# Kernel optimization log

Measured on AMD Instinct MI355X. Metric: run time of the kernel, lower is better.

Reference implementation:

```python
import jax, jax.numpy as jnp
import numpy as np

IN_CH = 4096
OUT_CH = 4096
NNZ = 838860
BATCH = 16384


def setup_inputs() -> dict:
    key = jax.random.key(0)
    k_x, k_w, k_b, k_r, k_c = jax.random.split(key, 5)
    x = jax.random.normal(k_x, (BATCH, IN_CH), dtype=jnp.float32)
    sparse_weight = jax.random.normal(k_w, (NNZ,), dtype=jnp.float32)
    bias = jax.random.normal(k_b, (OUT_CH,), dtype=jnp.float32)
    rows = jax.random.randint(k_r, (NNZ,), 0, OUT_CH, dtype=jnp.int32)
    cols = jax.random.randint(k_c, (NNZ,), 0, IN_CH, dtype=jnp.int32)
    return {"x": x, "sparse_weight": sparse_weight, "bias": bias, "rows": rows, "cols": cols}


def reference(x, sparse_weight, bias, rows, cols):
    # Scatter sparse weights into dense [OUT_CH, IN_CH] buffer (zero elsewhere),
    # exactly mirroring the torch module's per-call zero-fill + fancy-index assign.
    dense_weight = jnp.zeros((OUT_CH, IN_CH), dtype=sparse_weight.dtype)
    dense_weight = dense_weight.at[rows, cols].set(sparse_weight)
    # (W @ x.T).T + b  ==  x @ W.T + b
    return jnp.einsum('ni,oi->no', x, dense_weight) + bias
```

## Files before the change

kernel.cpp:

```cpp
#include <hip/hip_runtime.h>

#define IN_CH 4096
#define OUT_CH 4096
#define BATCH 16384

typedef __attribute__((ext_vector_type(8))) short bf16x8;
typedef __attribute__((ext_vector_type(4))) float f32x4;
typedef __attribute__((ext_vector_type(8))) unsigned short us8;

__device__ __forceinline__ unsigned short f2bf(float f) {
    union { float f; unsigned int u; } v; v.f = f;
    unsigned int u = v.u;
    unsigned int r = (u + 0x7fffu + ((u >> 16) & 1u)) >> 16;
    return (unsigned short)r;
}

__global__ void scatter_max(const int* __restrict__ rows, const int* __restrict__ cols,
                            int* __restrict__ idx, int nnz) {
    int i = blockIdx.x * blockDim.x + threadIdx.x;
    if (i < nnz) {
        atomicMax(&idx[(size_t)rows[i] * IN_CH + cols[i]], i + 1);
    }
}

__global__ void scatter_write(const int* __restrict__ rows, const int* __restrict__ cols,
                              const float* __restrict__ w, const int* __restrict__ idx,
                              unsigned short* __restrict__ W, int nnz) {
    int i = blockIdx.x * blockDim.x + threadIdx.x;
    if (i < nnz) {
        size_t cell = (size_t)rows[i] * IN_CH + cols[i];
        if (idx[cell] == i + 1) W[cell] = f2bf(w[i]);
    }
}

__global__ void convert_x(const float* __restrict__ x, unsigned short* __restrict__ xb) {
    size_t i = ((size_t)blockIdx.x * blockDim.x + threadIdx.x) * 8;
    float4 f0 = *(const float4*)(x + i);
    float4 f1 = *(const float4*)(x + i + 4);
    us8 o;
    o[0] = f2bf(f0.x); o[1] = f2bf(f0.y); o[2] = f2bf(f0.z); o[3] = f2bf(f0.w);
    o[4] = f2bf(f1.x); o[5] = f2bf(f1.y); o[6] = f2bf(f1.z); o[7] = f2bf(f1.w);
    *(us8*)(xb + i) = o;
}

__device__ __forceinline__ void gl_lds16(const unsigned short* g, unsigned short* l) {
    __builtin_amdgcn_global_load_lds(
        (const __attribute__((address_space(1))) unsigned int*)g,
        (__attribute__((address_space(3))) unsigned int*)l,
        16, 0, 0);
}

__global__ __launch_bounds__(256) void gemm_bt(
    const unsigned short* __restrict__ A,
    const unsigned short* __restrict__ B,
    const float* __restrict__ bias,
    float* __restrict__ C)
{
    __shared__ unsigned short lds[8192];
    const int tid  = threadIdx.x;
    const int wave = tid >> 6;
    const int lane = tid & 63;
    const int bm = blockIdx.x >> 5;
    const int bn = blockIdx.x & 31;
    const int wm = wave & 1;
    const int wn = wave >> 1;
    const int ml   = lane & 15;
    const int quad = lane >> 4;
    const int srow = lane >> 2;
    const int c    = lane & 3;
    const int scol = (c ^ ((srow >> 1) & 3)) * 8;

    const int seg0 = wave * 2;
    const unsigned short* ga0 = A + (size_t)(bm * 128 + seg0 * 16 + srow) * IN_CH + scol;
    const unsigned short* ga1 = ga0 + 16 * IN_CH;
    const unsigned short* gb0 = B + (size_t)(bn * 128 + seg0 * 16 + srow) * IN_CH + scol;
    const unsigned short* gb1 = gb0 + 16 * IN_CH;
    unsigned short* la0 = lds + seg0 * 512;
    unsigned short* la1 = la0 + 512;
    unsigned short* lb0 = lds + 4096 + seg0 * 512;
    unsigned short* lb1 = lb0 + 512;

    f32x4 acc[4][4];
#pragma unroll
    for (int i = 0; i < 4; ++i)
#pragma unroll
        for (int j = 0; j < 4; ++j) acc[i][j] = (f32x4){0.f, 0.f, 0.f, 0.f};

    const unsigned short* ldsA = lds;
    const unsigned short* ldsB = lds + 4096;
    const int swk = (quad ^ ((ml >> 1) & 3)) * 8;

    for (int kt = 0; kt < IN_CH / 32; ++kt) {
        gl_lds16(ga0, la0);
        gl_lds16(ga1, la1);
        gl_lds16(gb0, lb0);
        gl_lds16(gb1, lb1);
        __syncthreads();

        bf16x8 af[4], bf[4];
#pragma unroll
        for (int mt = 0; mt < 4; ++mt)
            af[mt] = *(const bf16x8*)(ldsA + (size_t)(wm * 64 + mt * 16 + ml) * 32 + swk);
#pragma unroll
        for (int nt = 0; nt < 4; ++nt)
            bf[nt] = *(const bf16x8*)(ldsB + (size_t)(wn * 64 + nt * 16 + ml) * 32 + swk);

#pragma unroll
        for (int mt = 0; mt < 4; ++mt)
#pragma unroll
            for (int nt = 0; nt < 4; ++nt)
                acc[mt][nt] = __builtin_amdgcn_mfma_f32_16x16x32_bf16(
                    af[mt], bf[nt], acc[mt][nt], 0, 0, 0);

        __syncthreads();
        ga0 += 32; ga1 += 32; gb0 += 32; gb1 += 32;
    }

    const int gm0 = bm * 128 + wm * 64;
    const int gn0 = bn * 128 + wn * 64;
#pragma unroll
    for (int nt = 0; nt < 4; ++nt) {
        const int gn = gn0 + nt * 16 + ml;
        const float bv = bias[gn];
#pragma unroll
        for (int mt = 0; mt < 4; ++mt) {
            const int gm = gm0 + mt * 16 + quad * 4;
#pragma unroll
            for (int r = 0; r < 4; ++r)
                C[(size_t)(gm + r) * OUT_CH + gn] = acc[mt][nt][r] + bv;
        }
    }
}

extern "C" void kernel_launch(void* const* d_in, const int* in_sizes, int n_in,
                              void* d_out, int out_size, void* d_ws, size_t ws_size,
                              hipStream_t stream) {
    const float* x    = (const float*)d_in[0];
    const float* sw   = (const float*)d_in[1];
    const float* bias = (const float*)d_in[2];
    const int*   rows = (const int*)d_in[3];
    const int*   cols = (const int*)d_in[4];
    const int    nnz  = in_sizes[1];

    char* base = (char*)d_ws;
    unsigned short* W  = (unsigned short*)base;
    int*            idx = (int*)(base + (size_t)OUT_CH * IN_CH * 2);
    unsigned short* xb  = (unsigned short*)(base + (size_t)OUT_CH * IN_CH * 2);

    hipMemsetAsync(d_ws, 0, (size_t)OUT_CH * IN_CH * 2 + (size_t)OUT_CH * IN_CH * 4, stream);
    hipLaunchKernelGGL(scatter_max, dim3((nnz + 255) / 256), dim3(256), 0, stream,
                       rows, cols, idx, nnz);
    hipLaunchKernelGGL(scatter_write, dim3((nnz + 255) / 256), dim3(256), 0, stream,
                       rows, cols, sw, idx, W, nnz);
    hipLaunchKernelGGL(convert_x, dim3(32768), dim3(256), 0, stream, x, xb);
    hipLaunchKernelGGL(gemm_bt, dim3(4096), dim3(256), 0, stream, xb, W, bias, (float*)d_out);
}
```

Before: 1.112 ms.

## Rewrite GEMM as 256x256-tile, 8-wave, double-buffered ping-pong pipeline

Replaces the 128x128 single-buffer GEMM with 256x256 tiles, 512 threads, and 64-wide K steps double-buffered in LDS. Global-to-LDS loads for the next stage are interleaved with MFMA quadrants under explicit barriers and vmcnt waits, MFMA issue priority is raised with setprio, and blocks are swizzled for L2 reuse. The aim is to hide memory latency, cut sync stalls and raise arithmetic intensity. It costs more LDS and registers per block and depends on a delicate hand-written barrier schedule.

```diff
diff --git a/kernel.cpp b/kernel.cpp
--- a/kernel.cpp
+++ b/kernel.cpp
@@ -50,84 +50,198 @@
         16, 0, 0);
 }
 
-__global__ __launch_bounds__(256) void gemm_bt(
+#define BAR()   asm volatile("s_barrier" ::: "memory")
+#define LGKM0() asm volatile("s_waitcnt lgkmcnt(0)" ::: "memory")
+#define VMC(n)  asm volatile("s_waitcnt vmcnt(" #n ")" ::: "memory")
+
+#define STAGE_A(gsrc, ldst) do {                                            \
+    gl_lds16((gsrc) + gAoff, ldsA_w + (ldst));                              \
+    gl_lds16((gsrc) + gAoff + (size_t)128 * IN_CH, ldsA_w + (ldst) + 8192); \
+} while (0)
+
+#define STAGE_B(gsrc, ldst) do {                                            \
+    gl_lds16((gsrc) + gBoff, ldsB_w + (ldst));                              \
+    gl_lds16((gsrc) + gBoff + (size_t)128 * IN_CH, ldsB_w + (ldst) + 8192); \
+} while (0)
+
+#define LD_A(dst, bufbase, mh) do { _Pragma("unroll")                       \
+    for (int mt = 0; mt < 4; ++mt) {                                        \
+        dst[mt][0] = *(const bf16x8*)(lds + (bufbase) + (mh)*4096 + aRow + mt*1024 + axk0); \
+        dst[mt][1] = *(const bf16x8*)(lds + (bufbase) + (mh)*4096 + aRow + mt*1024 + axk1); \
+    } } while (0)
+
+#define LD_B(dst, bufbase, nh) do { _Pragma("unroll")                       \
+    for (int nt = 0; nt < 2; ++nt) {                                        \
+        dst[nt][0] = *(const bf16x8*)(lds + (bufbase) + (nh)*2048 + bRow + nt*1024 + axk0); \
+        dst[nt][1] = *(const bf16x8*)(lds + (bufbase) + (nh)*2048 + bRow + nt*1024 + axk1); \
+    } } while (0)
+
+#define MFMA_Q(mh, nh, aF, bF) do {                                         \
+    __builtin_amdgcn_s_setprio(1);                                          \
+    _Pragma("unroll") for (int mt = 0; mt < 4; ++mt)                        \
+    _Pragma("unroll") for (int nt = 0; nt < 2; ++nt)                        \
+    _Pragma("unroll") for (int kk = 0; kk < 2; ++kk)                        \
+        acc[(mh)*4+mt][(nh)*2+nt] = __builtin_amdgcn_mfma_f32_16x16x32_bf16( \
+            aF[mt][kk], bF[nt][kk], acc[(mh)*4+mt][(nh)*2+nt], 0, 0, 0);    \
+    __builtin_amdgcn_s_setprio(0);                                          \
+} while (0)
+
+__global__ __launch_bounds__(512, 2) void gemm_bt(
     const unsigned short* __restrict__ A,
     const unsigned short* __restrict__ B,
     const float* __restrict__ bias,
     float* __restrict__ C)
 {
-    __shared__ unsigned short lds[8192];
+    __shared__ unsigned short lds[65536];
     const int tid  = threadIdx.x;
     const int wave = tid >> 6;
     const int lane = tid & 63;
-    const int bm = blockIdx.x >> 5;
-    const int bn = blockIdx.x & 31;
-    const int wm = wave & 1;
-    const int wn = wave >> 1;
     const int ml   = lane & 15;
     const int quad = lane >> 4;
-    const int srow = lane >> 2;
-    const int c    = lane & 3;
-    const int scol = (c ^ ((srow >> 1) & 3)) * 8;
-
-    const int seg0 = wave * 2;
-    const unsigned short* ga0 = A + (size_t)(bm * 128 + seg0 * 16 + srow) * IN_CH + scol;
-    const unsigned short* ga1 = ga0 + 16 * IN_CH;
-    const unsigned short* gb0 = B + (size_t)(bn * 128 + seg0 * 16 + srow) * IN_CH + scol;
-    const unsigned short* gb1 = gb0 + 16 * IN_CH;
-    unsigned short* la0 = lds + seg0 * 512;
-    unsigned short* la1 = la0 + 512;
-    unsigned short* lb0 = lds + 4096 + seg0 * 512;
-    unsigned short* lb1 = lb0 + 512;
-
-    f32x4 acc[4][4];
-#pragma unroll
-    for (int i = 0; i < 4; ++i)
+    const int wm   = wave >> 2;
+    const int wn   = wave & 3;
+
+    const int swz = (blockIdx.x & 7) * 128 + (blockIdx.x >> 3);
+    const int bm = swz >> 4;
+    const int bn = swz & 15;
+
+    const int lrow = lane >> 3;
+    const int lchk = (lane & 7) ^ lrow;
+    const int rA = wave * 8;
+    const int rB = (wave & 3) * 8 + (wave >> 2) * 64;
+    const size_t gAoff = (size_t)(rA + lrow) * IN_CH + lchk * 8;
+    const size_t gBoff = (size_t)(rB + lrow) * IN_CH + lchk * 8;
+    unsigned short* ldsA_w = lds + rA * 64;
+    unsigned short* ldsB_w = lds + rB * 64;
+
+    const unsigned short* gA = A + (size_t)bm * 256 * IN_CH;
+    const unsigned short* gB = B + (size_t)bn * 256 * IN_CH;
+
+    const int axk0 = ((quad)     ^ (ml & 7)) * 8;
+    const int axk1 = ((quad ^ 4) ^ (ml & 7)) * 8;
+    const int aRow = (wm * 128 + ml) * 64;
+    const int bRow = (wn * 64  + ml) * 64;
+
+    f32x4 acc[8][4];
+#pragma unroll
+    for (int i = 0; i < 8; ++i)
 #pragma unroll
         for (int j = 0; j < 4; ++j) acc[i][j] = (f32x4){0.f, 0.f, 0.f, 0.f};
 
-    const unsigned short* ldsA = lds;
-    const unsigned short* ldsB = lds + 4096;
-    const int swk = (quad ^ ((ml >> 1) & 3)) * 8;
-
-    for (int kt = 0; kt < IN_CH / 32; ++kt) {
-        gl_lds16(ga0, la0);
-        gl_lds16(ga1, la1);
-        gl_lds16(gb0, lb0);
-        gl_lds16(gb1, lb1);
-        __syncthreads();
-
-        bf16x8 af[4], bf[4];
-#pragma unroll
-        for (int mt = 0; mt < 4; ++mt)
-            af[mt] = *(const bf16x8*)(ldsA + (size_t)(wm * 64 + mt * 16 + ml) * 32 + swk);
-#pragma unroll
-        for (int nt = 0; nt < 4; ++nt)
-            bf[nt] = *(const bf16x8*)(ldsB + (size_t)(wn * 64 + nt * 16 + ml) * 32 + swk);
-
-#pragma unroll
-        for (int mt = 0; mt < 4; ++mt)
-#pragma unroll
-            for (int nt = 0; nt < 4; ++nt)
-                acc[mt][nt] = __builtin_amdgcn_mfma_f32_16x16x32_bf16(
-                    af[mt], bf[nt], acc[mt][nt], 0, 0, 0);
-
-        __syncthreads();
-        ga0 += 32; ga1 += 32; gb0 += 32; gb1 += 32;
-    }
-
-    const int gm0 = bm * 128 + wm * 64;
-    const int gn0 = bn * 128 + wn * 64;
-#pragma unroll
-    for (int nt = 0; nt < 4; ++nt) {
-        const int gn = gn0 + nt * 16 + ml;
+    bf16x8 aL[4][2], aH[4][2], bL[2][2], bH[2][2];
+    const bf16x8 zf = (bf16x8){0, 0, 0, 0, 0, 0, 0, 0};
+#pragma unroll
+    for (int mt = 0; mt < 4; ++mt) { aH[mt][0] = zf; aH[mt][1] = zf; }
+#pragma unroll
+    for (int nt = 0; nt < 2; ++nt) { bH[nt][0] = zf; bH[nt][1] = zf; }
+
+    STAGE_A(gA,                            0);
+    STAGE_B(gB,                            16384);
+    STAGE_A(gA + (size_t)64 * IN_CH,       4096);
+    STAGE_B(gB + (size_t)32 * IN_CH,       16384 + 2048);
+    STAGE_A(gA + 64,                       32768);
+    STAGE_B(gB + 64,                       32768 + 16384);
+    STAGE_A(gA + 64 + (size_t)64 * IN_CH,  32768 + 4096);
+    VMC(6);
+    BAR();
+
+#pragma unroll 1
+    for (int i = 0; i < 31; ++i) {
+        const size_t k2i = (size_t)i * 128;
+
+        LD_A(aL, 0, 0);
+        STAGE_B(gB + k2i + 64 + (size_t)32 * IN_CH, 32768 + 16384 + 2048);
+        BAR(); LGKM0();
+        MFMA_Q(1, 1, aH, bH);
+        BAR();
+        LD_B(bL, 16384, 0);
+        STAGE_A(gA + k2i + 128, 0);
+        BAR(); LGKM0();
+        MFMA_Q(0, 0, aL, bL);
+        BAR();
+        LD_A(aH, 0, 1);
+        STAGE_B(gB + k2i + 128, 16384);
+        BAR(); LGKM0();
+        MFMA_Q(1, 0, aH, bL);
+        BAR();
+        LD_B(bH, 16384, 1);
+        STAGE_A(gA + k2i + 128 + (size_t)64 * IN_CH, 4096);
+        VMC(6);
+        BAR(); LGKM0();
+        MFMA_Q(0, 1, aL, bH);
+        BAR();
+        LD_A(aL, 32768, 0);
+        STAGE_B(gB + k2i + 128 + (size_t)32 * IN_CH, 16384 + 2048);
+        BAR(); LGKM0();
+        MFMA_Q(1, 1, aH, bH);
+        BAR();
+        LD_B(bL, 32768 + 16384, 0);
+        STAGE_A(gA + k2i + 192, 32768);
+        BAR(); LGKM0();
+        MFMA_Q(0, 0, aL, bL);
+        BAR();
+        LD_A(aH, 32768, 1);
+        STAGE_B(gB + k2i + 192, 32768 + 16384);
+        BAR(); LGKM0();
+        MFMA_Q(1, 0, aH, bL);
+        BAR();
+        LD_B(bH, 32768 + 16384, 1);
+        STAGE_A(gA + k2i + 192 + (size_t)64 * IN_CH, 32768 + 4096);
+        VMC(6);
+        BAR(); LGKM0();
+        MFMA_Q(0, 1, aL, bH);
+        BAR();
+    }
+
+    {
+        LD_A(aL, 0, 0);
+        STAGE_B(gB + 4032 + (size_t)32 * IN_CH, 32768 + 16384 + 2048);
+        BAR(); LGKM0();
+        MFMA_Q(1, 1, aH, bH);
+        BAR();
+        LD_B(bL, 16384, 0);
+        BAR(); LGKM0();
+        MFMA_Q(0, 0, aL, bL);
+        BAR();
+        LD_A(aH, 0, 1);
+        BAR(); LGKM0();
+        MFMA_Q(1, 0, aH, bL);
+        BAR();
+        LD_B(bH, 16384, 1);
+        VMC(0);
+        BAR(); LGKM0();
+        MFMA_Q(0, 1, aL, bH);
+        BAR();
+        LD_A(aL, 32768, 0);
+        BAR(); LGKM0();
+        MFMA_Q(1, 1, aH, bH);
+        BAR();
+        LD_B(bL, 32768 + 16384, 0);
+        BAR(); LGKM0();
+        MFMA_Q(0, 0, aL, bL);
+        BAR();
+        LD_A(aH, 32768, 1);
+        BAR(); LGKM0();
+        MFMA_Q(1, 0, aH, bL);
+        BAR();
+        LD_B(bH, 32768 + 16384, 1);
+        LGKM0();
+        MFMA_Q(0, 1, aL, bH);
+        MFMA_Q(1, 1, aH, bH);
+    }
+
+    const int gm0 = bm * 256 + wm * 128;
+    const int gn0 = bn * 256 + wn * 64;
+#pragma unroll
+    for (int nf = 0; nf < 4; ++nf) {
+        const int gn = gn0 + nf * 16 + ml;
         const float bv = bias[gn];
 #pragma unroll
-        for (int mt = 0; mt < 4; ++mt) {
-            const int gm = gm0 + mt * 16 + quad * 4;
+        for (int mf = 0; mf < 8; ++mf) {
+            const int gm = gm0 + mf * 16 + quad * 4;
 #pragma unroll
             for (int r = 0; r < 4; ++r)
-                C[(size_t)(gm + r) * OUT_CH + gn] = acc[mt][nt][r] + bv;
+                C[(size_t)(gm + r) * OUT_CH + gn] = acc[mf][nf][r] + bv;
         }
     }
 }
@@ -153,5 +267,5 @@
     hipLaunchKernelGGL(scatter_write, dim3((nnz + 255) / 256), dim3(256), 0, stream,
                        rows, cols, sw, idx, W, nnz);
     hipLaunchKernelGGL(convert_x, dim3(32768), dim3(256), 0, stream, x, xb);
-    hipLaunchKernelGGL(gemm_bt, dim3(4096), dim3(256), 0, stream, xb, W, bias, (float*)d_out);
-}
+    hipLaunchKernelGGL(gemm_bt, dim3(1024), dim3(512), 0, stream, xb, W, bias, (float*)d_out);
+}
```

Result: faster. 910.2 us (-18.1%).
